# Kernel tuning notes

Measured on AMD Instinct MI355X. Metric: run time of the kernel, lower is better.

## Reference

```python
import jax, jax.numpy as jnp
import numpy as np
import math

LMAX = 2
NUM_RBF = 32
CUTOFF = 5.0
MUL_EDGE = 4          # mul_per_l
N_NODES = 50000
N_EDGES = 800000
NODE_MULS = [64, 32, 16]   # multiplicities of 0e,1o,2e in node_irreps
MSG_MULS = [64, 32, 16]    # multiplicities of 0e,1o,2e in msg_irreps
NODE_DIM = sum(m * (2 * l + 1) for l, m in enumerate(NODE_MULS))  # 240
# parity-conserving CG paths (l1 from node, l2 from edge, l3 to msg)
PATHS = [(0,0,0),(1,1,0),(2,2,0),(0,1,1),(1,0,1),(1,2,1),(2,1,1),(0,2,2),(2,0,2),(1,1,2),(2,2,2)]
TP_SIZES = [NODE_MULS[l1]*MUL_EDGE*MSG_MULS[l3] for (l1,l2,l3) in PATHS]
FAN_IN = {l3: sum(NODE_MULS[p1]*MUL_EDGE for (p1,p2,p3) in PATHS if p3 == l3) for l3 in range(LMAX+1)}


def _su2_cg(j1, m1, j2, m2, j3, m3):
    # Racah formula for SU(2) Clebsch-Gordan coefficients (integer l)
    if m3 != m1 + m2:
        return 0.0
    f = lambda n: math.factorial(int(n))
    vmin = int(max(-j1 + j2 + m3, -j1 + m1, 0))
    vmax = int(min(j2 + j3 + m1, j3 - j1 + j2, j3 + m3))
    C = math.sqrt((2*j3+1) * f(j3+j1-j2) * f(j3-j1+j2) * f(j1+j2-j3) * f(j3+m3) * f(j3-m3)
                  / (f(j1+j2+j3+1) * f(j1-m1) * f(j1+m1) * f(j2-m2) * f(j2+m2)))
    S = 0.0
    for v in range(vmin, vmax+1):
        S += (-1.0)**(v + j2 + m2) * f(j2+j3+m1-v) * f(j1-m1+v) / (
            f(v) * f(j3-j1+j2-v) * f(j3+m3-v) * f(v+j1-j2-m3))
    return C * S


def _real_to_complex(l):
    # change of basis real spherical harmonics -> complex, with phase making 3j real
    q = np.zeros((2*l+1, 2*l+1), dtype=np.complex128)
    for m in range(-l, 0):
        q[l+m, l+abs(m)] = 1/math.sqrt(2)
        q[l+m, l-abs(m)] = -1j/math.sqrt(2)
    q[l, l] = 1.0
    for m in range(1, l+1):
        q[l+m, l+abs(m)] = (-1)**m / math.sqrt(2)
        q[l+m, l-abs(m)] = 1j*(-1)**m / math.sqrt(2)
    return (-1j)**l * q


def _wigner_3j(l1, l2, l3):
    C = np.zeros((2*l1+1, 2*l2+1, 2*l3+1))
    for m1 in range(-l1, l1+1):
        for m2 in range(-l2, l2+1):
            for m3 in range(-l3, l3+1):
                C[l1+m1, l2+m2, l3+m3] = _su2_cg(l1, m1, l2, m2, l3, m3)
    Q1, Q2, Q3 = _real_to_complex(l1), _real_to_complex(l2), _real_to_complex(l3)
    Cc = np.einsum('ij,kl,mn,ikn->jlm', Q1, Q2, np.conj(Q3).T, C.astype(np.complex128))
    Cr = np.real(Cc)
    if np.linalg.norm(Cr) < 1e-8:
        Cr = np.imag(Cc)
    return (Cr / np.linalg.norm(Cr)).astype(np.float32)

W3J = {p: jnp.asarray(_wigner_3j(*p)) for p in PATHS}


def setup_inputs() -> dict:
    key = jax.random.key(0)
    ks = jax.random.split(key, 8)
    node_feat = jax.random.normal(ks[0], (N_NODES, NODE_DIM), jnp.float32)
    edge_index = jax.random.randint(ks[1], (2, N_EDGES), 0, N_NODES)
    edge_vec = jax.random.normal(ks[2], (N_EDGES, 3), jnp.float32) * 1.5
    mask = jax.random.uniform(ks[3], (N_EDGES,), jnp.float32)
    mlp_w1 = jax.random.normal(ks[4], (LMAX+1, NUM_RBF, 32), jnp.float32) / math.sqrt(NUM_RBF)
    mlp_b1 = jnp.zeros((LMAX+1, 32), jnp.float32)
    mlp_w2 = jax.random.normal(ks[5], (LMAX+1, 32, MUL_EDGE), jnp.float32) / math.sqrt(32.0)
    mlp_b2 = jnp.zeros((LMAX+1, MUL_EDGE), jnp.float32)
    tp_w = jax.random.normal(ks[6], (sum(TP_SIZES),), jnp.float32)
    return {"node_feat": node_feat, "edge_index": edge_index, "edge_vec": edge_vec,
            "mask": mask, "mlp_w1": mlp_w1, "mlp_b1": mlp_b1,
            "mlp_w2": mlp_w2, "mlp_b2": mlp_b2, "tp_w": tp_w}


def reference(node_feat, edge_index, edge_vec, mask, mlp_w1, mlp_b1, mlp_w2, mlp_b2, tp_w):
    src = edge_index[0]
    r = jnp.maximum(jnp.linalg.norm(edge_vec, axis=-1, keepdims=True), 1e-12)   # [E,1]
    r_hat = edge_vec / r
    x, y, z = r_hat[:, 0], r_hat[:, 1], r_hat[:, 2]
    # --- RBFEmb (smooth cosine cutoff + gaussians in exp(-r) space), then the
    # extra rbounds factor applied again in _edge_features (faithful to source)
    rbounds = 0.5 * (jnp.cos(r * jnp.pi / CUTOFF) + 1.0)                         # [E,1]
    means = jnp.linspace(math.exp(-CUTOFF), 1.0, NUM_RBF).astype(edge_vec.dtype)
    beta = (2.0 / NUM_RBF * (1.0 - math.exp(-CUTOFF))) ** (-2)
    rbf = rbounds * (r < CUTOFF).astype(edge_vec.dtype) * jnp.exp(-beta * jnp.square(jnp.exp(-r) - means))
    rbf = rbounds * rbf                                                          # [E,NUM_RBF]
    # --- real spherical harmonics, e3nn 'component' normalization, l = 0,1,2
    s3, s5, s15 = math.sqrt(3.0), math.sqrt(5.0), math.sqrt(15.0)
    Y = [jnp.ones_like(x)[:, None],
         s3 * r_hat,
         jnp.stack([s15 * x * z, s15 * x * y, s5 * (y * y - 0.5 * (x * x + z * z)),
                    s15 * y * z, 0.5 * s15 * (z * z - x * x)], axis=-1)]
    # --- per-l radial MLP weights, outer product with Y_l -> edge irrep blocks
    edge_blocks = []
    for l in range(LMAX + 1):
        h = jax.nn.silu(rbf @ mlp_w1[l] + mlp_b1[l])
        w_l = h @ mlp_w2[l] + mlp_b2[l]                                          # [E,MUL_EDGE]
        edge_blocks.append(w_l[:, :, None] * Y[l][:, None, :])                   # [E,MUL_EDGE,2l+1]
    # --- gather node features per edge and split into irrep blocks
    f_i = node_feat[src]                                                         # [E,NODE_DIM]
    node_blocks, off = [], 0
    for l, mul in enumerate(NODE_MULS):
        d = mul * (2 * l + 1)
        node_blocks.append(f_i[:, off:off + d].reshape(-1, mul, 2 * l + 1))
        off += d
    # --- fully-connected CG tensor product (per-path small contractions)
    terms = {l3: [] for l3 in range(LMAX + 1)}
    woff = 0
    for (l1, l2, l3), sz in zip(PATHS, TP_SIZES):
        W = tp_w[woff:woff + sz].reshape(NODE_MULS[l1], MUL_EDGE, MSG_MULS[l3])
        woff += sz
        alpha = 1.0 / math.sqrt(FAN_IN[l3])
        terms[l3].append(alpha * jnp.einsum('eui,evj,uvw,ijk->ewk',
                                            node_blocks[l1], edge_blocks[l2], W,
                                            W3J[(l1, l2, l3)], optimize='optimal'))
    E = edge_vec.shape[0]
    msg_e = jnp.concatenate([sum(terms[l3]).reshape(E, -1) for l3 in range(LMAX + 1)], axis=-1)
    return msg_e * mask[:, None]
```

## Files before the change

### kernel.cpp

```cpp
#include <hip/hip_runtime.h>
#include <math.h>

#define TE 32
#define NODE_DIM 240
#define NPAD 248

typedef _Float16 f16;
typedef f16 f16x2 __attribute__((ext_vector_type(2)));
typedef f16 f16x4 __attribute__((ext_vector_type(4)));
typedef f16 f16x8 __attribute__((ext_vector_type(8)));
typedef float f32x4 __attribute__((ext_vector_type(4)));


struct cplx { double re, im; };
__device__ inline cplx cmul(cplx a, cplx b) {
    return { a.re*b.re - a.im*b.im, a.re*b.im + a.im*b.re };
}

__device__ double dfact(int n) { double r = 1.0; for (int i = 2; i <= n; ++i) r *= i; return r; }

__device__ double su2_cg(int j1, int m1, int j2, int m2, int j3, int m3) {
    if (m3 != m1 + m2) return 0.0;
    int vmin = max(max(-j1 + j2 + m3, -j1 + m1), 0);
    int vmax = min(min(j2 + j3 + m1, j3 - j1 + j2), j3 + m3);
    double C = sqrt((2.0*j3 + 1.0) * dfact(j3 + j1 - j2) * dfact(j3 - j1 + j2) * dfact(j1 + j2 - j3)
                    * dfact(j3 + m3) * dfact(j3 - m3)
                    / (dfact(j1 + j2 + j3 + 1) * dfact(j1 - m1) * dfact(j1 + m1)
                       * dfact(j2 - m2) * dfact(j2 + m2)));
    double S = 0.0;
    for (int v = vmin; v <= vmax; ++v) {
        double sgn = ((v + j2 + m2) & 1) ? -1.0 : 1.0;
        S += sgn * dfact(j2 + j3 + m1 - v) * dfact(j1 - m1 + v)
             / (dfact(v) * dfact(j3 - j1 + j2 - v) * dfact(j3 + m3 - v) * dfact(v + j1 - j2 - m3));
    }
    return C * S;
}

__device__ cplx rtc(int l, int a, int b) {
    double re = 0.0, im = 0.0;
    const double inv_s2 = 0.70710678118654752440;
    int m = a - l;
    if (m < 0) {
        if (b == l - m)      re = inv_s2;
        else if (b == l + m) im = -inv_s2;
    } else if (m == 0) {
        if (b == l) re = 1.0;
    } else {
        double s = (m & 1) ? -1.0 : 1.0;
        if (b == l + m)      re = s * inv_s2;
        else if (b == l - m) im = s * inv_s2;
    }
    if (l == 1) { double t = re; re = im; im = -t; }
    else if (l == 2) { re = -re; im = -im; }
    return { re, im };
}

__global__ void w3j_init(float* __restrict__ out) {
    __shared__ double sRe[363], sIm[363];
    __shared__ double sNorm[11];
    __shared__ int    sUse[11];
    const int L1A[11] = {0,1,2,0,1,1,2,0,2,1,2};
    const int L2A[11] = {0,1,2,1,0,2,1,2,0,1,2};
    const int L3A[11] = {0,0,0,1,1,1,1,2,2,2,2};
    const int OFF[12] = {0,1,10,35,44,53,98,143,168,193,238,363};
    int t = threadIdx.x;
    if (t < 363) {
        int p = 0;
        while (p < 10 && t >= OFF[p+1]) ++p;
        int rel = t - OFF[p];
        int a1 = L1A[p], a2 = L2A[p], a3 = L3A[p];
        int n1 = 2*a1 + 1, n2 = 2*a2 + 1, n3 = 2*a3 + 1;
        int jj = rel / (n2*n3), ll = (rel / n3) % n2, mm = rel % n3;
        double cr = 0.0, ci = 0.0;
        for (int i = 0; i < n1; ++i)
            for (int k = 0; k < n2; ++k)
                for (int n = 0; n < n3; ++n) {
                    double c = su2_cg(a1, i - a1, a2, k - a2, a3, n - a3);
                    if (c == 0.0) continue;
                    cplx q1 = rtc(a1, i, jj);
                    cplx q2 = rtc(a2, k, ll);
                    cplx q3 = rtc(a3, n, mm); q3.im = -q3.im;
                    cplx pr = cmul(cmul(q1, q2), q3);
                    cr += pr.re * c; ci += pr.im * c;
                }
        sRe[t] = cr; sIm[t] = ci;
    }
    __syncthreads();
    if (t < 11) {
        double nr = 0.0, ni = 0.0;
        for (int e = OFF[t]; e < OFF[t+1]; ++e) { nr += sRe[e]*sRe[e]; ni += sIm[e]*sIm[e]; }
        int use_im = (sqrt(nr) < 1e-8) ? 1 : 0;
        sUse[t] = use_im;
        sNorm[t] = sqrt(use_im ? ni : nr);
    }
    __syncthreads();
    if (t < 363) {
        int p = 0;
        while (p < 10 && t >= OFF[p+1]) ++p;
        out[t] = (float)((sUse[p] ? sIm[t] : sRe[t]) / sNorm[p]);
    }
}

__global__ void w_prep(const float* __restrict__ tp_w, f16* __restrict__ wpre) {
    const int WOFF[11] = {0,16384,24576,28672,36864,40960,45056,47104,51200,52224,54272};
    const int UA[11]   = {64,32,16,64,32,32,16,64,16,32,16};
    const int NA[11]   = {64,64,64,32,32,32,32,16,16,16,16};
    const int L3A[11]  = {0,0,0,1,1,1,1,2,2,2,2};
    const float alph[3] = { 1.0f/sqrtf(448.0f), 1.0f/24.0f, 1.0f/sqrtf(512.0f) };
    int tid = threadIdx.x;
    for (int p = 0; p < 11; ++p) {
        int U = UA[p], N = NA[p], woff = WOFF[p];
        int NT = N/16;
        int size = U*4*N;
        float alpha = alph[L3A[p]];
        for (int j = tid; j < size; j += 256) {
            int f = j >> 9, r = j & 511;
            int lane = r >> 3, jj = r & 7;
            int ks = f / NT, nt = f - ks*NT;
            int k = ks*32 + (lane>>4)*8 + jj;
            int n = nt*16 + (lane&15);
            wpre[woff + j] = (f16)(tp_w[woff + k*N + n] * alpha);
        }
    }
}

template<int l1, int l2, int l3>
__device__ __forceinline__ void path_mfma(
    int tid, int woff, int cgoff,
    const f16* __restrict__ wpre,
    const f16* sN16, const float (*sY)[8], const float* sW3,
    const f16x2 (*sWlPk)[6],
    f32x4 (&acc)[3])
{
    constexpr int U  = (l1 == 0) ? 64 : (l1 == 1) ? 32 : 16;
    constexpr int N  = (l3 == 0) ? 64 : (l3 == 1) ? 32 : 16;
    constexpr int NI = 2*l1 + 1, NJ = 2*l2 + 1, NK = 2*l3 + 1;
    constexpr int M  = NK * TE;
    constexpr int NODE_OFF = (l1 == 0) ? 0 : (l1 == 1) ? 64 : 160;
    constexpr int KS = U / 8;
    constexpr int NT = N / 16;
    constexpr int NTASKS = (M/16) * NT;

    const int wv = tid >> 6, lane = tid & 63;
    const int ln = tid & 15, qt = (tid & 63) >> 4;

    #pragma unroll
    for (int t = 0; t < 3; ++t) {
        int task = t*4 + wv;
        if (task < NTASKS) {
            int mt = task / NT, nt = task - mt*NT;
            int row = mt*16 + ln;
            int e = row & 31, kk = row >> 5;
            float cyr[NI];
            #pragma unroll
            for (int i = 0; i < NI; ++i) {
                float c = 0.f;
                #pragma unroll
                for (int j = 0; j < NJ; ++j) {
                    float yj = (l2 == 0) ? 1.f : ((l2 == 1) ? sY[e][j] : sY[e][3 + j]);
                    c += sW3[cgoff + (i*NJ + j)*NK + kk] * yj;
                }
                cyr[i] = c;
            }
            f16x2 wl0 = sWlPk[e][l2*2 + 0];
            f16x2 wl1 = sWlPk[e][l2*2 + 1];
            const f16* nbase = sN16 + e*NPAD + NODE_OFF;
            const f16* wbase = wpre + woff + (size_t)nt*512 + lane*8;
            #pragma unroll
            for (int ks = 0; ks < KS; ++ks) {
                f16x8 wf = *(const f16x8*)(wbase + (size_t)ks*NT*512);
                int u0 = ks*8 + qt*2;
                float b0 = 0.f, b1 = 0.f;
                #pragma unroll
                for (int i = 0; i < NI; ++i) {
                    b0 += (float)nbase[u0*NI + i]      * cyr[i];
                    b1 += (float)nbase[u0*NI + NI + i] * cyr[i];
                }
                f16 b0h = (f16)b0, b1h = (f16)b1;
                f16x2 bb0 = {b0h, b0h}, bb1 = {b1h, b1h};
                f16x2 a01 = bb0*wl0, a23 = bb0*wl1, a45 = bb1*wl0, a67 = bb1*wl1;
                f16x8 af = {a01[0],a01[1],a23[0],a23[1],a45[0],a45[1],a67[0],a67[1]};
                acc[t] = __builtin_amdgcn_mfma_f32_16x16x32_f16(af, wf, acc[t], 0, 0, 0);
            }
        }
    }
}

template<int NK, int NT, int NTASKS, int OFF>
__device__ __forceinline__ void store_group(int tid, const f32x4 (&acc)[3], f16* sAcc16)
{
    int wv = tid >> 6;
    int ln = tid & 15, qt = (tid & 63) >> 4;
    #pragma unroll
    for (int t = 0; t < 3; ++t) {
        int task = t*4 + wv;
        if (task < NTASKS) {
            int mt = task / NT, nt = task % NT;
            int kk = mt >> 1;
            int e0 = (mt & 1) * 16;
            #pragma unroll
            for (int r = 0; r < 4; ++r) {
                int e = e0 + qt*4 + r;
                sAcc16[e*240 + OFF + (nt*16 + ln)*NK + kk] = (f16)acc[t][r];
            }
        }
    }
}

__global__ __launch_bounds__(256, 4)
void edge_main(const float* __restrict__ node_feat,
               const int*   __restrict__ edge_src,
               const float* __restrict__ edge_vec,
               const float* __restrict__ maskp,
               const float* __restrict__ mlp_w1, const float* __restrict__ mlp_b1,
               const float* __restrict__ mlp_w2, const float* __restrict__ mlp_b2,
               const f16*   __restrict__ wpre,
               const float* __restrict__ w3j,
               float* __restrict__ out)
{
    __shared__ __align__(16) f16 sN16[TE*NPAD];
    __shared__ __align__(16) f16 sAcc16[TE*240];
    __shared__ float sW3[364];
    __shared__ float sY[TE][8];
    __shared__ f16x2 sWlPk[TE][6];

    float* sRbf  = (float*)sAcc16;
    float* sH    = sRbf + TE*32;
    float* sWl   = sH   + TE*32;
    float* sR    = sWl  + TE*12;
    float* sRb2  = sR   + TE;
    float* sMask = sRb2 + TE;
    int*   sSrc  = (int*)(sMask + TE);

    int tid = threadIdx.x;
    long eg0 = (long)blockIdx.x * TE;

    if (tid < TE) {
        long eg = eg0 + tid;
        float vx = edge_vec[eg*3 + 0], vy = edge_vec[eg*3 + 1], vz = edge_vec[eg*3 + 2];
        float rn = sqrtf(vx*vx + vy*vy + vz*vz);
        float r  = fmaxf(rn, 1e-12f);
        float inv = 1.0f / r;
        float x = vx*inv, y = vy*inv, z = vz*inv;
        sR[tid] = r;
        float rb = 0.5f * (cosf(r * 3.14159265358979323846f / 5.0f) + 1.0f);
        sRb2[tid] = (r < 5.0f) ? rb*rb : 0.0f;
        sMask[tid] = maskp[eg];
        sSrc[tid]  = edge_src[eg];
        const float s3 = sqrtf(3.0f), s5 = sqrtf(5.0f), s15 = sqrtf(15.0f);
        sY[tid][0] = s3*x; sY[tid][1] = s3*y; sY[tid][2] = s3*z;
        sY[tid][3] = s15*x*z;
        sY[tid][4] = s15*x*y;
        sY[tid][5] = s5*(y*y - 0.5f*(x*x + z*z));
        sY[tid][6] = s15*y*z;
        sY[tid][7] = 0.5f*s15*(z*z - x*x);
    }
    for (int t = tid; t < 363; t += 256) sW3[t] = w3j[t];
    __syncthreads();

    {
        float em5  = expf(-5.0f);
        float step = (1.0f - em5) / 31.0f;
        float beta = 256.0f / ((1.0f - em5) * (1.0f - em5));
        for (int idx = tid; idx < TE*32; idx += 256) {
            int e = idx >> 5, j = idx & 31;
            float mean = em5 + step * j;
            float d = expf(-sR[e]) - mean;
            sRbf[e*32 + j] = sRb2[e] * expf(-beta * d * d);
        }
    }
    for (int idx = tid; idx < TE*60; idx += 256) {
        int e = idx / 60, q = idx - e*60;
        f32x4 v = *(const f32x4*)(node_feat + (long)sSrc[e]*NODE_DIM + q*4);
        f16x4 h = {(f16)v.x, (f16)v.y, (f16)v.z, (f16)v.w};
        *(f16x4*)&sN16[e*NPAD + q*4] = h;
    }
    __syncthreads();

    for (int l = 0; l < 3; ++l) {
        for (int idx = tid; idx < TE*32; idx += 256) {
            int e = idx >> 5, j = idx & 31;
            float zacc = mlp_b1[l*32 + j];
            #pragma unroll 8
            for (int rr = 0; rr < 32; ++rr) zacc += sRbf[e*32 + rr] * mlp_w1[(l*32 + rr)*32 + j];
            sH[e*32 + j] = zacc / (1.0f + expf(-zacc));
        }
        __syncthreads();
        for (int idx = tid; idx < TE*4; idx += 256) {
            int e = idx >> 2, v = idx & 3;
            float zacc = mlp_b2[l*4 + v];
            #pragma unroll 8
            for (int j = 0; j < 32; ++j) zacc += sH[e*32 + j] * mlp_w2[(l*32 + j)*4 + v];
            sWl[e*12 + l*4 + v] = zacc;
        }
        __syncthreads();
    }
    for (int idx = tid; idx < TE*6; idx += 256) {
        int e = idx / 6, h = idx - e*6;
        int l = h >> 1, vh = h & 1;
        float m = sMask[e];
        f16x2 p = {(f16)(sWl[e*12 + l*4 + vh*2] * m), (f16)(sWl[e*12 + l*4 + vh*2 + 1] * m)};
        sWlPk[e][h] = p;
    }
    __syncthreads();

    f32x4 acc[3];

    #pragma unroll
    for (int t = 0; t < 3; ++t) acc[t] = {0.f, 0.f, 0.f, 0.f};
    path_mfma<0,0,0>(tid,     0,   0, wpre, sN16, sY, sW3, sWlPk, acc);
    path_mfma<1,1,0>(tid, 16384,   1, wpre, sN16, sY, sW3, sWlPk, acc);
    path_mfma<2,2,0>(tid, 24576,  10, wpre, sN16, sY, sW3, sWlPk, acc);
    store_group<1, 4, 8, 0>(tid, acc, sAcc16);

    #pragma unroll
    for (int t = 0; t < 3; ++t) acc[t] = {0.f, 0.f, 0.f, 0.f};
    path_mfma<0,1,1>(tid, 28672,  35, wpre, sN16, sY, sW3, sWlPk, acc);
    path_mfma<1,0,1>(tid, 36864,  44, wpre, sN16, sY, sW3, sWlPk, acc);
    path_mfma<1,2,1>(tid, 40960,  53, wpre, sN16, sY, sW3, sWlPk, acc);
    path_mfma<2,1,1>(tid, 45056,  98, wpre, sN16, sY, sW3, sWlPk, acc);
    store_group<3, 2, 12, 64>(tid, acc, sAcc16);

    #pragma unroll
    for (int t = 0; t < 3; ++t) acc[t] = {0.f, 0.f, 0.f, 0.f};
    path_mfma<0,2,2>(tid, 47104, 143, wpre, sN16, sY, sW3, sWlPk, acc);
    path_mfma<2,0,2>(tid, 51200, 168, wpre, sN16, sY, sW3, sWlPk, acc);
    path_mfma<1,1,2>(tid, 52224, 193, wpre, sN16, sY, sW3, sWlPk, acc);
    path_mfma<2,2,2>(tid, 54272, 238, wpre, sN16, sY, sW3, sWlPk, acc);
    store_group<5, 1, 10, 160>(tid, acc, sAcc16);

    __syncthreads();

    for (int idx = tid; idx < TE*30; idx += 256) {
        int e = idx / 30, q = idx - e*30;
        f16x8 v = *(const f16x8*)&sAcc16[e*240 + q*8];
        f32x4 lo = {(float)v[0], (float)v[1], (float)v[2], (float)v[3]};
        f32x4 hi = {(float)v[4], (float)v[5], (float)v[6], (float)v[7]};
        float* dst = out + (eg0 + e)*NODE_DIM + q*8;
        __builtin_nontemporal_store(lo, (f32x4*)dst);
        __builtin_nontemporal_store(hi, (f32x4*)(dst + 4));
    }
}

extern "C" void kernel_launch(void* const* d_in, const int* in_sizes, int n_in,
                              void* d_out, int out_size, void* d_ws, size_t ws_size,
                              hipStream_t stream)
{
    const float* node_feat = (const float*)d_in[0];
    const int*   edge_idx  = (const int*)  d_in[1];
    const float* edge_vec  = (const float*)d_in[2];
    const float* maskp     = (const float*)d_in[3];
    const float* mlp_w1    = (const float*)d_in[4];
    const float* mlp_b1    = (const float*)d_in[5];
    const float* mlp_w2    = (const float*)d_in[6];
    const float* mlp_b2    = (const float*)d_in[7];
    const float* tp_w      = (const float*)d_in[8];
    float* out  = (float*)d_out;
    float* w3j  = (float*)d_ws;
    f16*   wpre = (f16*)((char*)d_ws + 2048);

    int E = in_sizes[3];
    const int* edge_src = edge_idx;

    hipLaunchKernelGGL(w3j_init, dim3(1), dim3(512), 0, stream, w3j);
    hipLaunchKernelGGL(w_prep,   dim3(1), dim3(256), 0, stream, tp_w, wpre);
    hipLaunchKernelGGL(edge_main, dim3(E / TE), dim3(256), 0, stream,
                       node_feat, edge_src, edge_vec, maskp,
                       mlp_w1, mlp_b1, mlp_w2, mlp_b2, wpre, w3j, out);
}
```

Measured before the change: 1.173 ms.

## Halve edge tile to 16 and interleave MFMA tasks across K-steps

Shrinks the per-block edge tile from 32 to 16 edges, so each MFMA row tile maps directly to one edge. The task mapping is simplified accordingly and the launch bound is raised to 8 blocks per SM to increase occupancy. The path loop is restructured to precompute the CG-Y coefficients for all of a wave's tasks and then iterate K-steps in the outer loop, which allows weight loads for several tasks to be issued together. Trade-off: each block reloads the weight matrix for only half as many edges, which doubles total weight traffic from L2. It also adds a cvtpk helper that nothing calls.

After: 1.984 ms. 69.2% more time.

```diff
diff --git a/kernel.cpp b/kernel.cpp
--- a/kernel.cpp
+++ b/kernel.cpp
@@ -1,7 +1,7 @@
 #include <hip/hip_runtime.h>
 #include <math.h>
 
-#define TE 32
+#define TE 16
 #define NODE_DIM 240
 #define NPAD 248
 
@@ -10,6 +10,14 @@
 typedef f16 f16x4 __attribute__((ext_vector_type(4)));
 typedef f16 f16x8 __attribute__((ext_vector_type(8)));
 typedef float f32x4 __attribute__((ext_vector_type(4)));
+
+__device__ __forceinline__ f16x2 cvtpk(float a, float b) {
+#if __has_builtin(__builtin_amdgcn_cvt_pkrtz)
+    return __builtin_bit_cast(f16x2, __builtin_amdgcn_cvt_pkrtz(a, b));
+#else
+    f16x2 r = {(f16)a, (f16)b}; return r;
+#endif
+}
 
 
 struct cplx { double re, im; };
@@ -130,28 +138,32 @@
     const f16* __restrict__ wpre,
     const f16* sN16, const float (*sY)[8], const float* sW3,
     const f16x2 (*sWlPk)[6],
-    f32x4 (&acc)[3])
+    f32x4 (&acc)[2])
 {
     constexpr int U  = (l1 == 0) ? 64 : (l1 == 1) ? 32 : 16;
     constexpr int N  = (l3 == 0) ? 64 : (l3 == 1) ? 32 : 16;
     constexpr int NI = 2*l1 + 1, NJ = 2*l2 + 1, NK = 2*l3 + 1;
-    constexpr int M  = NK * TE;
-    constexpr int NODE_OFF = (l1 == 0) ? 0 : (l1 == 1) ? 64 : 160;
+    constexpr int SEC = (l1 == 0) ? 0 : (l1 == 1) ? 64 : 160;
     constexpr int KS = U / 8;
     constexpr int NT = N / 16;
-    constexpr int NTASKS = (M/16) * NT;
+    constexpr int NTASKS = NK * NT;
+    constexpr int NW = (NTASKS + 3) / 4;
 
     const int wv = tid >> 6, lane = tid & 63;
     const int ln = tid & 15, qt = (tid & 63) >> 4;
-
-    #pragma unroll
-    for (int t = 0; t < 3; ++t) {
+    const int e = ln;
+
+    const f16* nb = sN16 + e*NPAD + SEC;
+    float cyT[NW][NI];
+    f16x2 wl0 = sWlPk[e][l2*2 + 0];
+    f16x2 wl1 = sWlPk[e][l2*2 + 1];
+    int ntT[NW];
+    #pragma unroll
+    for (int t = 0; t < NW; ++t) {
         int task = t*4 + wv;
         if (task < NTASKS) {
-            int mt = task / NT, nt = task - mt*NT;
-            int row = mt*16 + ln;
-            int e = row & 31, kk = row >> 5;
-            float cyr[NI];
+            int kk = task / NT;
+            ntT[t] = task % NT;
             #pragma unroll
             for (int i = 0; i < NI; ++i) {
                 float c = 0.f;
@@ -160,25 +172,30 @@
                     float yj = (l2 == 0) ? 1.f : ((l2 == 1) ? sY[e][j] : sY[e][3 + j]);
                     c += sW3[cgoff + (i*NJ + j)*NK + kk] * yj;
                 }
-                cyr[i] = c;
+                cyT[t][i] = c;
             }
-            f16x2 wl0 = sWlPk[e][l2*2 + 0];
-            f16x2 wl1 = sWlPk[e][l2*2 + 1];
-            const f16* nbase = sN16 + e*NPAD + NODE_OFF;
-            const f16* wbase = wpre + woff + (size_t)nt*512 + lane*8;
-            #pragma unroll
-            for (int ks = 0; ks < KS; ++ks) {
-                f16x8 wf = *(const f16x8*)(wbase + (size_t)ks*NT*512);
-                int u0 = ks*8 + qt*2;
+        }
+    }
+
+    #pragma unroll
+    for (int ks = 0; ks < KS; ++ks) {
+        const int u0 = ks*8 + qt*2;
+        #pragma unroll
+        for (int t = 0; t < NW; ++t) {
+            int task = t*4 + wv;
+            if (task < NTASKS) {
+                f16x8 wf = *(const f16x8*)(wpre + woff
+                            + (size_t)(ks*NT + ntT[t])*512 + lane*8);
                 float b0 = 0.f, b1 = 0.f;
                 #pragma unroll
                 for (int i = 0; i < NI; ++i) {
-                    b0 += (float)nbase[u0*NI + i]      * cyr[i];
-                    b1 += (float)nbase[u0*NI + NI + i] * cyr[i];
+                    b0 += (float)nb[u0*NI + i]      * cyT[t][i];
+                    b1 += (float)nb[u0*NI + NI + i] * cyT[t][i];
                 }
                 f16 b0h = (f16)b0, b1h = (f16)b1;
-                f16x2 bb0 = {b0h, b0h}, bb1 = {b1h, b1h};
-                f16x2 a01 = bb0*wl0, a23 = bb0*wl1, a45 = bb1*wl0, a67 = bb1*wl1;
+                f16x2 b00 = {b0h, b0h}, b11 = {b1h, b1h};
+                f16x2 a01 = b00*wl0, a23 = b00*wl1;
+                f16x2 a45 = b11*wl0, a67 = b11*wl1;
                 f16x8 af = {a01[0],a01[1],a23[0],a23[1],a45[0],a45[1],a67[0],a67[1]};
                 acc[t] = __builtin_amdgcn_mfma_f32_16x16x32_f16(af, wf, acc[t], 0, 0, 0);
             }
@@ -187,27 +204,26 @@
 }
 
 template<int NK, int NT, int NTASKS, int OFF>
-__device__ __forceinline__ void store_group(int tid, const f32x4 (&acc)[3], f16* sAcc16)
+__device__ __forceinline__ void store_group(int tid, const f32x4 (&acc)[2], f16* sAcc16)
 {
     int wv = tid >> 6;
     int ln = tid & 15, qt = (tid & 63) >> 4;
     #pragma unroll
-    for (int t = 0; t < 3; ++t) {
+    for (int t = 0; t < 2; ++t) {
         int task = t*4 + wv;
         if (task < NTASKS) {
-            int mt = task / NT, nt = task % NT;
-            int kk = mt >> 1;
-            int e0 = (mt & 1) * 16;
+            int kk = task / NT, nt = task % NT;
+            int ch = OFF + (nt*16 + ln)*NK + kk;
             #pragma unroll
             for (int r = 0; r < 4; ++r) {
-                int e = e0 + qt*4 + r;
-                sAcc16[e*240 + OFF + (nt*16 + ln)*NK + kk] = (f16)acc[t][r];
+                int e = qt*4 + r;
+                sAcc16[e*240 + ch] = (f16)acc[t][r];
             }
         }
     }
 }
 
-__global__ __launch_bounds__(256, 4)
+__global__ __launch_bounds__(256, 8)
 void edge_main(const float* __restrict__ node_feat,
                const int*   __restrict__ edge_src,
                const float* __restrict__ edge_vec,
@@ -304,30 +320,30 @@
     }
     __syncthreads();
 
-    f32x4 acc[3];
-
-    #pragma unroll
-    for (int t = 0; t < 3; ++t) acc[t] = {0.f, 0.f, 0.f, 0.f};
+    f32x4 acc[2];
+
+    #pragma unroll
+    for (int t = 0; t < 2; ++t) acc[t] = {0.f, 0.f, 0.f, 0.f};
     path_mfma<0,0,0>(tid,     0,   0, wpre, sN16, sY, sW3, sWlPk, acc);
     path_mfma<1,1,0>(tid, 16384,   1, wpre, sN16, sY, sW3, sWlPk, acc);
     path_mfma<2,2,0>(tid, 24576,  10, wpre, sN16, sY, sW3, sWlPk, acc);
-    store_group<1, 4, 8, 0>(tid, acc, sAcc16);
-
-    #pragma unroll
-    for (int t = 0; t < 3; ++t) acc[t] = {0.f, 0.f, 0.f, 0.f};
+    store_group<1, 4, 4, 0>(tid, acc, sAcc16);
+
+    #pragma unroll
+    for (int t = 0; t < 2; ++t) acc[t] = {0.f, 0.f, 0.f, 0.f};
     path_mfma<0,1,1>(tid, 28672,  35, wpre, sN16, sY, sW3, sWlPk, acc);
     path_mfma<1,0,1>(tid, 36864,  44, wpre, sN16, sY, sW3, sWlPk, acc);
     path_mfma<1,2,1>(tid, 40960,  53, wpre, sN16, sY, sW3, sWlPk, acc);
     path_mfma<2,1,1>(tid, 45056,  98, wpre, sN16, sY, sW3, sWlPk, acc);
-    store_group<3, 2, 12, 64>(tid, acc, sAcc16);
-
-    #pragma unroll
-    for (int t = 0; t < 3; ++t) acc[t] = {0.f, 0.f, 0.f, 0.f};
+    store_group<3, 2, 6, 64>(tid, acc, sAcc16);
+
+    #pragma unroll
+    for (int t = 0; t < 2; ++t) acc[t] = {0.f, 0.f, 0.f, 0.f};
     path_mfma<0,2,2>(tid, 47104, 143, wpre, sN16, sY, sW3, sWlPk, acc);
     path_mfma<2,0,2>(tid, 51200, 168, wpre, sN16, sY, sW3, sWlPk, acc);
     path_mfma<1,1,2>(tid, 52224, 193, wpre, sN16, sY, sW3, sWlPk, acc);
     path_mfma<2,2,2>(tid, 54272, 238, wpre, sN16, sY, sW3, sWlPk, acc);
-    store_group<5, 1, 10, 160>(tid, acc, sAcc16);
+    store_group<5, 1, 5, 160>(tid, acc, sAcc16);
 
     __syncthreads();
 
```
